# Kernel optimization log

Hardware: AMD Instinct MI355X
Metric: run time of the kernel (lower is better)

## Reference

```python
import jax, jax.numpy as jnp
import numpy as np

DIM = 512
HEADS = 8
DIM_HEAD = 64
INNER = HEADS * DIM_HEAD  # 512
B, N = 4, 2048


def setup_inputs() -> dict:
    key = jax.random.key(0)
    k1, k2, k3, k4 = jax.random.split(key, 4)
    x = jax.random.normal(k1, (B, N, DIM), dtype=jnp.float32)
    # nn.Linear(dim, inner*3, bias=False): weight [3*inner, dim]; store transposed [dim, 3*inner]
    w_qkv = jax.random.normal(k2, (DIM, 3 * INNER), dtype=jnp.float32) / np.sqrt(DIM)
    w_out = jax.random.normal(k3, (INNER, DIM), dtype=jnp.float32) / np.sqrt(INNER)
    b_out = jax.random.normal(k4, (DIM,), dtype=jnp.float32) * 0.01
    return {"x": x, "w_qkv": w_qkv, "w_out": w_out, "b_out": b_out}


def reference(x, w_qkv, w_out, b_out):
    b, n, _ = x.shape
    scale = DIM_HEAD ** -0.5
    qkv = x @ w_qkv  # [b, n, 3*inner]
    q, k, v = jnp.split(qkv, 3, axis=-1)
    # [b, n, h, d] -> [b, h, n, d]
    reshape = lambda t: t.reshape(b, n, HEADS, DIM_HEAD).transpose(0, 2, 1, 3)
    q, k, v = reshape(q), reshape(k), reshape(v)
    dots = jnp.einsum('bhid,bhjd->bhij', q, k) * scale  # [b, h, n, n]
    attn = jax.nn.softmax(dots, axis=-1)
    out = jnp.einsum('bhij,bhjd->bhid', attn, v)  # [b, h, n, d]
    out = out.transpose(0, 2, 1, 3).reshape(b, n, INNER)
    return out @ w_out + b_out  # dropout is identity at inference
```

## Files before the change

### kernel.cpp

```cpp
#include <hip/hip_runtime.h>
#include <hip/hip_bf16.h>
#include <cstdint>

#define DEV __device__ __forceinline__

typedef __attribute__((ext_vector_type(8))) __bf16 bf16x8;
typedef __attribute__((ext_vector_type(4))) float floatx4;
typedef __attribute__((ext_vector_type(4))) short shortx4;
typedef __attribute__((ext_vector_type(8))) short shortx8;

constexpr float QSCALE = 0.18033688011112042f;

DEV unsigned short f2b(float f) {
  union { float f; unsigned u; } v; v.f = f;
  return (unsigned short)((v.u + 0x7fffu + ((v.u >> 16) & 1u)) >> 16);
}

#if defined(__has_builtin) && __has_builtin(__builtin_amdgcn_cvt_pk_bf16_f32)
DEV unsigned pk2(float a, float b) {
  typedef __attribute__((ext_vector_type(2))) __bf16 bf2;
  union { bf2 v; unsigned u; } u;
  u.v = __builtin_amdgcn_cvt_pk_bf16_f32(a, b);
  return u.u;
}
#else
DEV unsigned pk2(float a, float b) {
  return (unsigned)f2b(a) | ((unsigned)f2b(b) << 16);
}
#endif

#if defined(__has_builtin) && __has_builtin(__builtin_amdgcn_exp2f)
DEV float fexp2(float x) { return __builtin_amdgcn_exp2f(x); }
#else
DEV float fexp2(float x) { return exp2f(x); }
#endif

DEV floatx4 mfma16(bf16x8 a, bf16x8 b, floatx4 c) {
  return __builtin_amdgcn_mfma_f32_16x16x32_bf16(a, b, c, 0, 0, 0);
}

#define GLD_LDS16(gp, lp)                                                          \
  __builtin_amdgcn_global_load_lds(                                                \
      (const __attribute__((address_space(1))) void*)(gp),                         \
      (__attribute__((address_space(3))) void*)(lp), 16, 0, 0)

__global__ void cvt_f32_bf16(const float* __restrict__ in,
                             unsigned short* __restrict__ out, int n4) {
  int i = blockIdx.x * 256 + threadIdx.x;
  if (i >= n4) return;
  floatx4 f = ((const floatx4*)in)[i];
  shortx4 s;
  s[0] = (short)f2b(f[0]); s[1] = (short)f2b(f[1]);
  s[2] = (short)f2b(f[2]); s[3] = (short)f2b(f[3]);
  ((shortx4*)out)[i] = s;
}

__global__ void tcvt2(const float* __restrict__ w_qkv,
                      const float* __restrict__ w_out,
                      unsigned short* __restrict__ wqkvt,
                      unsigned short* __restrict__ woutt) {
  __shared__ float tile[32][33];
  const float* in; unsigned short* out; int C, bx;
  if (blockIdx.x < 48) { in = w_qkv; out = wqkvt; C = 1536; bx = blockIdx.x; }
  else { in = w_out; out = woutt; C = 512; bx = blockIdx.x - 48; }
  const int R = 512;
  int tx = threadIdx.x & 31, ty = threadIdx.x >> 5;
  int r0 = blockIdx.y * 32, c0 = bx * 32;
#pragma unroll
  for (int i = 0; i < 4; i++) {
    int rr = ty + i * 8;
    tile[rr][tx] = in[(size_t)(r0 + rr) * C + c0 + tx];
  }
  __syncthreads();
#pragma unroll
  for (int i = 0; i < 4; i++) {
    int rr = ty + i * 8;
    out[(size_t)(c0 + rr) * R + r0 + tx] = f2b(tile[tx][rr]);
  }
}

__global__ __launch_bounds__(256, 3) void gemm_qkv(
    const unsigned short* __restrict__ A, const unsigned short* __restrict__ Bt,
    unsigned short* __restrict__ qf, unsigned short* __restrict__ kg,
    unsigned short* __restrict__ vf) {
  __shared__ __align__(16) unsigned short smem[17408];
  const int tid = threadIdx.x;
  const int lane = tid & 63, wid = tid >> 6;
  const int g = lane >> 4, r = lane & 15;
  const int m0 = blockIdx.y * 128, n0 = blockIdx.x * 128;
  const int wm = (wid & 1) * 64, wn = (wid >> 1) * 64;
  const int K = 512;

  floatx4 acc[4][4] = {};

  int rowA[2], kbA[2];
#pragma unroll
  for (int i = 0; i < 2; i++) {
    int c = i * 256 + tid;
    rowA[i] = c >> 2;
    kbA[i] = (c & 3) ^ ((rowA[i] >> 1) & 3);
  }

#define STAGE_G(kt, b)                                                           \
  {                                                                              \
    _Pragma("unroll") for (int i = 0; i < 2; i++) {                              \
      GLD_LDS16(A + (size_t)(m0 + rowA[i]) * K + (kt) + kbA[i] * 8,              \
                (char*)smem + (b)*8192 + i * 4096 + wid * 1024);                 \
      GLD_LDS16(Bt + (size_t)(n0 + rowA[i]) * K + (kt) + kbA[i] * 8,             \
                (char*)smem + 16384 + (b)*8192 + i * 4096 + wid * 1024);         \
    }                                                                            \
  }

  STAGE_G(0, 0)
  for (int it = 0; it < 16; it++) {
    const int buf = it & 1;
    __syncthreads();
    if (it + 1 < 16) STAGE_G((it + 1) * 32, buf ^ 1)
    const unsigned short* Xs = smem + buf * 4096;
    const unsigned short* Ws = smem + 8192 + buf * 4096;
    bf16x8 a[4], b[4];
#pragma unroll
    for (int t = 0; t < 4; t++) {
      int rw = wm + t * 16 + r;
      a[t] = *(const bf16x8*)(Xs + rw * 32 + (g ^ ((rw >> 1) & 3)) * 8);
      int rb = wn + t * 16 + r;
      b[t] = *(const bf16x8*)(Ws + rb * 32 + (g ^ ((rb >> 1) & 3)) * 8);
    }
#pragma unroll
    for (int mt = 0; mt < 4; mt++)
#pragma unroll
      for (int nt = 0; nt < 4; nt++)
        acc[mt][nt] = mfma16(a[mt], b[nt], acc[mt][nt]);
  }
#undef STAGE_G

  const int which = blockIdx.x >> 2;
  if (which == 2) {
    const int tokbase = m0 + wm;
    const int bb = tokbase >> 11, vt = (tokbase & 2047) >> 6;
#pragma unroll
    for (int nt = 0; nt < 4; nt++) {
      int vcol = n0 + wn + nt * 16 + r - 1024;
      int h = vcol >> 6;
      size_t hb = (size_t)(bb * 8 + h) * 131072 + (size_t)vt * 4096 + nt * 1024 +
                  (g * 16 + r) * 8;
#pragma unroll
      for (int kc = 0; kc < 2; kc++) {
        union { unsigned u[4]; shortx8 v; } w;
        w.u[0] = pk2(acc[2 * kc][nt][0], acc[2 * kc][nt][1]);
        w.u[1] = pk2(acc[2 * kc][nt][2], acc[2 * kc][nt][3]);
        w.u[2] = pk2(acc[2 * kc + 1][nt][0], acc[2 * kc + 1][nt][1]);
        w.u[3] = pk2(acc[2 * kc + 1][nt][2], acc[2 * kc + 1][nt][3]);
        *(shortx8*)(vf + hb + kc * 512) = w.v;
      }
    }
  } else {
    const float sc = (which == 0) ? QSCALE : 1.f;
    __syncthreads();
#pragma unroll
    for (int mt = 0; mt < 4; mt++)
#pragma unroll
      for (int nt = 0; nt < 4; nt++) {
        int col = wn + nt * 16 + r;
#pragma unroll
        for (int e = 0; e < 4; e++)
          smem[(wm + mt * 16 + g * 4 + e) * 136 + col] = f2b(acc[mt][nt][e] * sc);
      }
    __syncthreads();
#pragma unroll
    for (int it = 0; it < 8; it++) {
      int c = it * 256 + tid;
      int row = c >> 4, cc = c & 15;
      shortx8 v = *(const shortx8*)(smem + row * 136 + cc * 8);
      int gq = n0 + cc * 8;
      int h = (gq >> 6) & 7, d0 = gq & 63;
      int tok = m0 + row, bb = tok >> 11, n = tok & 2047;
      if (which == 0) {
        int kc = d0 >> 5, gp = (d0 >> 3) & 3;
        *(shortx8*)(qf + (size_t)(bb * 8 + h) * 131072 + (n >> 4) * 1024 +
                    kc * 512 + (gp * 16 + (n & 15)) * 8) = v;
      } else {
        *(shortx8*)(kg + ((size_t)(bb * 8 + h) * 2048 + n) * 64 + d0) = v;
      }
    }
  }
}

__global__ __launch_bounds__(256, 2) void gemm_out(
    const unsigned short* __restrict__ A, const unsigned short* __restrict__ Bt,
    float* __restrict__ outF, const float* __restrict__ bias) {
  __shared__ __align__(16) unsigned short smem[16896];
  const int tid = threadIdx.x;
  const int lane = tid & 63, wid = tid >> 6;
  const int g = lane >> 4, r = lane & 15;
  const int m0 = blockIdx.y * 64, n0 = blockIdx.x * 128;
  const int wn = wid * 32;
  const int K = 512;

  floatx4 acc[4][2] = {};

  const int rA = tid >> 2, kA = (tid & 3) ^ ((rA >> 1) & 3);
  int rB[2], kB[2];
#pragma unroll
  for (int i = 0; i < 2; i++) {
    int c = i * 256 + tid;
    rB[i] = c >> 2;
    kB[i] = (c & 3) ^ ((rB[i] >> 1) & 3);
  }

#define STAGE_O(kt, b)                                                           \
  {                                                                              \
    GLD_LDS16(A + (size_t)(m0 + rA) * K + (kt) + kA * 8,                         \
              (char*)smem + (b)*4096 + wid * 1024);                              \
    _Pragma("unroll") for (int i = 0; i < 2; i++)                                \
        GLD_LDS16(Bt + (size_t)(n0 + rB[i]) * K + (kt) + kB[i] * 8,              \
                  (char*)smem + 8192 + (b)*8192 + i * 4096 + wid * 1024);        \
  }

  STAGE_O(0, 0)
  for (int it = 0; it < 16; it++) {
    const int buf = it & 1;
    __syncthreads();
    if (it + 1 < 16) STAGE_O((it + 1) * 32, buf ^ 1)
    const unsigned short* Xs = smem + buf * 2048;
    const unsigned short* Ws = smem + 4096 + buf * 4096;
    bf16x8 a[4], b[2];
#pragma unroll
    for (int t = 0; t < 4; t++) {
      int rw = t * 16 + r;
      a[t] = *(const bf16x8*)(Xs + rw * 32 + (g ^ ((rw >> 1) & 3)) * 8);
    }
#pragma unroll
    for (int t = 0; t < 2; t++) {
      int rb = wn + t * 16 + r;
      b[t] = *(const bf16x8*)(Ws + rb * 32 + (g ^ ((rb >> 1) & 3)) * 8);
    }
#pragma unroll
    for (int mt = 0; mt < 4; mt++)
#pragma unroll
      for (int bt = 0; bt < 2; bt++)
        acc[mt][bt] = mfma16(a[mt], b[bt], acc[mt][bt]);
  }
#undef STAGE_O

  float* ftile = (float*)smem;
  __syncthreads();
#pragma unroll
  for (int mt = 0; mt < 4; mt++)
#pragma unroll
    for (int bt = 0; bt < 2; bt++)
#pragma unroll
      for (int e = 0; e < 4; e++)
        ftile[(mt * 16 + g * 4 + e) * 132 + wn + bt * 16 + r] = acc[mt][bt][e];
  __syncthreads();
#pragma unroll
  for (int it = 0; it < 8; it++) {
    int c = it * 256 + tid;
    int lr = c >> 5, cc = c & 31;
    floatx4 v = *(const floatx4*)(ftile + lr * 132 + cc * 4);
    int col = n0 + cc * 4;
    v += *(const floatx4*)(bias + col);
    *(floatx4*)(outF + (size_t)(m0 + lr) * 512 + col) = v;
  }
}

__global__ __launch_bounds__(256, 2) void attn(
    const unsigned short* __restrict__ qf, const unsigned short* __restrict__ kg,
    const unsigned short* __restrict__ vf, unsigned short* __restrict__ ao) {
  __shared__ __align__(16) char L[65536];
  unsigned short* Ksm = (unsigned short*)L;
  const int tid = threadIdx.x, lane = tid & 63, wid = tid >> 6;
  const int g = lane >> 4, r = lane & 15, r7 = r & 7;
  const int wq = wid & 1, wk = wid >> 1;
  const int bh = blockIdx.y;
  const size_t kbase = (size_t)bh * (2048 * 64);
  const size_t fbase = (size_t)bh * 131072;
  const unsigned short* vb = vf + fbase;
  const int srow = lane >> 3;
  const int chunk = (lane & 7) ^ (srow & 7);

  const int qt0 = (blockIdx.x * 128 + wq * 64) >> 4;
  bf16x8 bq[4][2];
#pragma unroll
  for (int nt = 0; nt < 4; nt++)
#pragma unroll
    for (int kc = 0; kc < 2; kc++)
      bq[nt][kc] = *(const bf16x8*)(qf + fbase + (size_t)(qt0 + nt) * 1024 +
                                    kc * 512 + lane * 8);

  bf16x8 vones;
#pragma unroll
  for (int i = 0; i < 8; i++) vones[i] = (__bf16)1.0f;

  floatx4 o[4][4] = {};
  floatx4 lacc[4] = {};

#define STAGE_K(rnd, b)                                                          \
  {                                                                              \
    _Pragma("unroll") for (int j = 0; j < 8; j++) {                              \
      int row = (rnd)*256 + wid * 64 + j * 8 + srow;                             \
      GLD_LDS16(kg + kbase + (size_t)row * 64 + chunk * 8,                       \
                (char*)L + (b)*32768 + wid * 8192 + j * 1024);                   \
    }                                                                            \
  }

  STAGE_K(0, 0)
  for (int rnd = 0; rnd < 8; rnd++) {
    const int buf = rnd & 1;
    __syncthreads();
    if (rnd + 1 < 8) STAGE_K(rnd + 1, buf ^ 1)
    const unsigned short* Kt = Ksm + buf * 16384 + (wk * 128) * 64;
#pragma unroll
    for (int sub = 0; sub < 2; sub++) {
      const unsigned short* Ks_ = Kt + sub * 64 * 64;
      const int vt = (rnd * 256 + wk * 128 + sub * 64) >> 6;

      bf16x8 bv[4][2];
#pragma unroll
      for (int b = 0; b < 4; b++)
#pragma unroll
        for (int kc = 0; kc < 2; kc++)
          bv[b][kc] = *(const bf16x8*)(vb + (size_t)vt * 4096 + b * 1024 +
                                       kc * 512 + lane * 8);

      floatx4 st[4][4] = {};
#pragma unroll
      for (int kc = 0; kc < 2; kc++)
#pragma unroll
        for (int mt = 0; mt < 4; mt++) {
          bf16x8 ak = *(const bf16x8*)(Ks_ + (mt * 16 + r) * 64 +
                                       ((kc * 4 + g) ^ r7) * 8);
#pragma unroll
          for (int nt = 0; nt < 4; nt++)
            st[mt][nt] = mfma16(ak, bq[nt][kc], st[mt][nt]);
        }

      bf16x8 ap[4][2];
#pragma unroll
      for (int a = 0; a < 4; a++) {
        float p[4][4];
#pragma unroll
        for (int mt = 0; mt < 4; mt++)
#pragma unroll
          for (int e = 0; e < 4; e++) p[mt][e] = fexp2(st[mt][a][e]);
#pragma unroll
        for (int kc = 0; kc < 2; kc++) {
          union { unsigned u[4]; bf16x8 v; } w;
          w.u[0] = pk2(p[2 * kc][0], p[2 * kc][1]);
          w.u[1] = pk2(p[2 * kc][2], p[2 * kc][3]);
          w.u[2] = pk2(p[2 * kc + 1][0], p[2 * kc + 1][1]);
          w.u[3] = pk2(p[2 * kc + 1][2], p[2 * kc + 1][3]);
          ap[a][kc] = w.v;
        }
      }

#pragma unroll
      for (int kc = 0; kc < 2; kc++)
#pragma unroll
        for (int a = 0; a < 4; a++) {
          lacc[a] = mfma16(ap[a][kc], vones, lacc[a]);
#pragma unroll
          for (int b = 0; b < 4; b++)
            o[a][b] = mfma16(ap[a][kc], bv[b][kc], o[a][b]);
        }
    }
  }
#undef STAGE_K

  float* fP = (float*)L;
  float* fL = (float*)(L + 32768);
  unsigned short* Osm = (unsigned short*)(L + 40960);
  __syncthreads();
  if (wk == 1) {
#pragma unroll
    for (int a = 0; a < 4; a++) {
      *(floatx4*)&fL[wq * 1024 + a * 256 + lane * 4] = lacc[a];
#pragma unroll
      for (int b = 0; b < 4; b++)
        *(floatx4*)&fP[wq * 4096 + (a * 4 + b) * 256 + lane * 4] = o[a][b];
    }
  }
  __syncthreads();
  if (wk == 0) {
#pragma unroll
    for (int a = 0; a < 4; a++) {
      floatx4 lt = lacc[a] + *(floatx4*)&fL[wq * 1024 + a * 256 + lane * 4];
      floatx4 il;
#pragma unroll
      for (int e = 0; e < 4; e++) il[e] = 1.f / lt[e];
#pragma unroll
      for (int b = 0; b < 4; b++) {
        floatx4 oo = o[a][b] +
                     *(floatx4*)&fP[wq * 4096 + (a * 4 + b) * 256 + lane * 4];
#pragma unroll
        for (int e = 0; e < 4; e++)
          Osm[wq * 4608 + (a * 16 + g * 4 + e) * 72 + b * 16 + r] =
              f2b(oo[e] * il[e]);
      }
    }
  }
  __syncthreads();
  const int bb = bh >> 3, h = bh & 7;
#pragma unroll
  for (int it = 0; it < 4; it++) {
    int c = it * 256 + tid;
    int row = c >> 3, cc = c & 7;
    int wqi = row >> 6, r6 = row & 63;
    shortx8 v = *(const shortx8*)(Osm + wqi * 4608 + r6 * 72 + cc * 8);
    int tok = blockIdx.x * 128 + row;
    *(shortx8*)(ao + ((size_t)(bb * 2048 + tok)) * 512 + h * 64 + cc * 8) = v;
  }
}

extern "C" void kernel_launch(void* const* d_in, const int* in_sizes, int n_in,
                              void* d_out, int out_size, void* d_ws, size_t ws_size,
                              hipStream_t stream) {
  const float* x = (const float*)d_in[0];
  const float* w_qkv = (const float*)d_in[1];
  const float* w_out = (const float*)d_in[2];
  const float* b_out = (const float*)d_in[3];
  float* out = (float*)d_out;

  unsigned short* wsp = (unsigned short*)d_ws;
  unsigned short* xb = wsp;
  unsigned short* wqkvt = xb + (size_t)8192 * 512;
  unsigned short* woutt = wqkvt + (size_t)1536 * 512;
  unsigned short* qf = woutt + (size_t)512 * 512;
  unsigned short* kg = qf + (size_t)32 * 2048 * 64;
  unsigned short* vf = kg + (size_t)32 * 2048 * 64;
  unsigned short* ao = vf + (size_t)32 * 2048 * 64;

  cvt_f32_bf16<<<4096, 256, 0, stream>>>(x, xb, 8192 * 512 / 4);
  tcvt2<<<dim3(64, 16), 256, 0, stream>>>(w_qkv, w_out, wqkvt, woutt);
  gemm_qkv<<<dim3(12, 64), 256, 0, stream>>>(xb, wqkvt, qf, kg, vf);
  attn<<<dim3(16, 32), 256, 0, stream>>>(qf, kg, vf, ao);
  gemm_out<<<dim3(4, 128), 256, 0, stream>>>(ao, woutt, out, b_out);
}
```

Baseline: 153.8 us.

## Merge prep kernels, swizzle block order, and add MFMA priority hints in attention

Folds the x conversion and weight transpose kernels into a single prep launch, which drops one kernel launch. The QKV GEMM grid is remapped so consecutive blocks land on different XCDs, and the attention grid is flattened so each XCD gets a subset of heads, aiming at better per-XCD L2 reuse of K/V. Inside attention, the K/V pointers advance incrementally, the QK^T accumulation is restructured to start from zero per tile, and s_setprio wraps the MFMA bursts to favour matrix-op issue. The swizzle mappings must stay bijective, and the priority hints may or may not help scheduling.

```diff
diff --git a/kernel.cpp b/kernel.cpp
--- a/kernel.cpp
+++ b/kernel.cpp
@@ -44,28 +44,30 @@
       (const __attribute__((address_space(1))) void*)(gp),                         \
       (__attribute__((address_space(3))) void*)(lp), 16, 0, 0)
 
-__global__ void cvt_f32_bf16(const float* __restrict__ in,
-                             unsigned short* __restrict__ out, int n4) {
-  int i = blockIdx.x * 256 + threadIdx.x;
-  if (i >= n4) return;
-  floatx4 f = ((const floatx4*)in)[i];
-  shortx4 s;
-  s[0] = (short)f2b(f[0]); s[1] = (short)f2b(f[1]);
-  s[2] = (short)f2b(f[2]); s[3] = (short)f2b(f[3]);
-  ((shortx4*)out)[i] = s;
-}
-
-__global__ void tcvt2(const float* __restrict__ w_qkv,
-                      const float* __restrict__ w_out,
-                      unsigned short* __restrict__ wqkvt,
-                      unsigned short* __restrict__ woutt) {
+__global__ void prep(const float* __restrict__ x,
+                     const float* __restrict__ w_qkv,
+                     const float* __restrict__ w_out,
+                     unsigned short* __restrict__ xb,
+                     unsigned short* __restrict__ wqkvt,
+                     unsigned short* __restrict__ woutt) {
   __shared__ float tile[32][33];
+  if (blockIdx.x < 4096) {
+    int i = blockIdx.x * 256 + threadIdx.x;
+    floatx4 f = ((const floatx4*)x)[i];
+    shortx4 s;
+    s[0] = (short)f2b(f[0]); s[1] = (short)f2b(f[1]);
+    s[2] = (short)f2b(f[2]); s[3] = (short)f2b(f[3]);
+    ((shortx4*)xb)[i] = s;
+    return;
+  }
+  int id = blockIdx.x - 4096;
+  int bxr = id & 63, by = id >> 6;
   const float* in; unsigned short* out; int C, bx;
-  if (blockIdx.x < 48) { in = w_qkv; out = wqkvt; C = 1536; bx = blockIdx.x; }
-  else { in = w_out; out = woutt; C = 512; bx = blockIdx.x - 48; }
+  if (bxr < 48) { in = w_qkv; out = wqkvt; C = 1536; bx = bxr; }
+  else { in = w_out; out = woutt; C = 512; bx = bxr - 48; }
   const int R = 512;
   int tx = threadIdx.x & 31, ty = threadIdx.x >> 5;
-  int r0 = blockIdx.y * 32, c0 = bx * 32;
+  int r0 = by * 32, c0 = bx * 32;
 #pragma unroll
   for (int i = 0; i < 4; i++) {
     int rr = ty + i * 8;
@@ -87,7 +89,10 @@
   const int tid = threadIdx.x;
   const int lane = tid & 63, wid = tid >> 6;
   const int g = lane >> 4, r = lane & 15;
-  const int m0 = blockIdx.y * 128, n0 = blockIdx.x * 128;
+  const int flat = blockIdx.y * 12 + blockIdx.x;
+  const int sw = (flat & 7) * 96 + (flat >> 3);
+  const int bx = sw % 12, by = sw / 12;
+  const int m0 = by * 128, n0 = bx * 128;
   const int wm = (wid & 1) * 64, wn = (wid >> 1) * 64;
   const int K = 512;
 
@@ -134,7 +139,7 @@
   }
 #undef STAGE_G
 
-  const int which = blockIdx.x >> 2;
+  const int which = bx >> 2;
   if (which == 2) {
     const int tokbase = m0 + wm;
     const int bb = tokbase >> 11, vt = (tokbase & 2047) >> 6;
@@ -272,14 +277,15 @@
   const int tid = threadIdx.x, lane = tid & 63, wid = tid >> 6;
   const int g = lane >> 4, r = lane & 15, r7 = r & 7;
   const int wq = wid & 1, wk = wid >> 1;
-  const int bh = blockIdx.y;
+  const int slot = blockIdx.x;
+  const int bh = ((slot & 7) << 2) | ((slot >> 3) & 3);
+  const int qt = slot >> 5;
   const size_t kbase = (size_t)bh * (2048 * 64);
   const size_t fbase = (size_t)bh * 131072;
-  const unsigned short* vb = vf + fbase;
   const int srow = lane >> 3;
   const int chunk = (lane & 7) ^ (srow & 7);
 
-  const int qt0 = (blockIdx.x * 128 + wq * 64) >> 4;
+  const int qt0 = qt * 8 + wq * 4;
   bf16x8 bq[4][2];
 #pragma unroll
   for (int nt = 0; nt < 4; nt++)
@@ -291,49 +297,54 @@
   bf16x8 vones;
 #pragma unroll
   for (int i = 0; i < 8; i++) vones[i] = (__bf16)1.0f;
+  const floatx4 fzero = {0.f, 0.f, 0.f, 0.f};
 
   floatx4 o[4][4] = {};
   floatx4 lacc[4] = {};
 
-#define STAGE_K(rnd, b)                                                          \
+  const unsigned short* vbp = vf + fbase + (size_t)(wk * 2) * 4096 + lane * 8;
+  const unsigned short* kgp =
+      kg + kbase + (size_t)(wid * 64 + srow) * 64 + chunk * 8;
+
+#define STAGE_K(b)                                                               \
   {                                                                              \
     _Pragma("unroll") for (int j = 0; j < 8; j++) {                              \
-      int row = (rnd)*256 + wid * 64 + j * 8 + srow;                             \
-      GLD_LDS16(kg + kbase + (size_t)row * 64 + chunk * 8,                       \
-                (char*)L + (b)*32768 + wid * 8192 + j * 1024);                   \
+      GLD_LDS16(kgp + j * 512, (char*)L + (b)*32768 + wid * 8192 + j * 1024);    \
     }                                                                            \
-  }
-
-  STAGE_K(0, 0)
+    kgp += 16384;                                                                \
+  }
+
+  STAGE_K(0)
   for (int rnd = 0; rnd < 8; rnd++) {
     const int buf = rnd & 1;
     __syncthreads();
-    if (rnd + 1 < 8) STAGE_K(rnd + 1, buf ^ 1)
-    const unsigned short* Kt = Ksm + buf * 16384 + (wk * 128) * 64;
+    if (rnd + 1 < 8) STAGE_K(buf ^ 1)
+    const unsigned short* Kt = Ksm + buf * 16384 + wk * 8192;
 #pragma unroll
     for (int sub = 0; sub < 2; sub++) {
-      const unsigned short* Ks_ = Kt + sub * 64 * 64;
-      const int vt = (rnd * 256 + wk * 128 + sub * 64) >> 6;
+      const unsigned short* Ks_ = Kt + sub * 4096;
 
       bf16x8 bv[4][2];
 #pragma unroll
       for (int b = 0; b < 4; b++)
 #pragma unroll
         for (int kc = 0; kc < 2; kc++)
-          bv[b][kc] = *(const bf16x8*)(vb + (size_t)vt * 4096 + b * 1024 +
-                                       kc * 512 + lane * 8);
-
-      floatx4 st[4][4] = {};
-#pragma unroll
-      for (int kc = 0; kc < 2; kc++)
-#pragma unroll
-        for (int mt = 0; mt < 4; mt++) {
-          bf16x8 ak = *(const bf16x8*)(Ks_ + (mt * 16 + r) * 64 +
-                                       ((kc * 4 + g) ^ r7) * 8);
-#pragma unroll
-          for (int nt = 0; nt < 4; nt++)
-            st[mt][nt] = mfma16(ak, bq[nt][kc], st[mt][nt]);
+          bv[b][kc] = *(const bf16x8*)(vbp + sub * 4096 + b * 1024 + kc * 512);
+
+      floatx4 st[4][4];
+      __builtin_amdgcn_s_setprio(1);
+#pragma unroll
+      for (int mt = 0; mt < 4; mt++) {
+        bf16x8 ak0 = *(const bf16x8*)(Ks_ + (mt * 16 + r) * 64 + (g ^ r7) * 8);
+        bf16x8 ak1 =
+            *(const bf16x8*)(Ks_ + (mt * 16 + r) * 64 + ((4 + g) ^ r7) * 8);
+#pragma unroll
+        for (int nt = 0; nt < 4; nt++) {
+          floatx4 t = mfma16(ak0, bq[nt][0], fzero);
+          st[mt][nt] = mfma16(ak1, bq[nt][1], t);
         }
+      }
+      __builtin_amdgcn_s_setprio(0);
 
       bf16x8 ap[4][2];
 #pragma unroll
@@ -354,6 +365,7 @@
         }
       }
 
+      __builtin_amdgcn_s_setprio(1);
 #pragma unroll
       for (int kc = 0; kc < 2; kc++)
 #pragma unroll
@@ -363,7 +375,9 @@
           for (int b = 0; b < 4; b++)
             o[a][b] = mfma16(ap[a][kc], bv[b][kc], o[a][b]);
         }
-    }
+      __builtin_amdgcn_s_setprio(0);
+    }
+    vbp += 16384;
   }
 #undef STAGE_K
 
@@ -407,7 +421,7 @@
     int row = c >> 3, cc = c & 7;
     int wqi = row >> 6, r6 = row & 63;
     shortx8 v = *(const shortx8*)(Osm + wqi * 4608 + r6 * 72 + cc * 8);
-    int tok = blockIdx.x * 128 + row;
+    int tok = qt * 128 + row;
     *(shortx8*)(ao + ((size_t)(bb * 2048 + tok)) * 512 + h * 64 + cc * 8) = v;
   }
 }
@@ -430,9 +444,8 @@
   unsigned short* vf = kg + (size_t)32 * 2048 * 64;
   unsigned short* ao = vf + (size_t)32 * 2048 * 64;
 
-  cvt_f32_bf16<<<4096, 256, 0, stream>>>(x, xb, 8192 * 512 / 4);
-  tcvt2<<<dim3(64, 16), 256, 0, stream>>>(w_qkv, w_out, wqkvt, woutt);
+  prep<<<5120, 256, 0, stream>>>(x, w_qkv, w_out, xb, wqkvt, woutt);
   gemm_qkv<<<dim3(12, 64), 256, 0, stream>>>(xb, wqkvt, qf, kg, vf);
-  attn<<<dim3(16, 32), 256, 0, stream>>>(qf, kg, vf, ao);
+  attn<<<dim3(512), 256, 0, stream>>>(qf, kg, vf, ao);
   gemm_out<<<dim3(4, 128), 256, 0, stream>>>(ao, woutt, out, b_out);
 }
```

Measured after the change: 147.9 us. 1.04x faster.
